# Kernel tuning notes

Measured on AMD Instinct MI355X. Metric: run time of the kernel, lower is better.

The kernel has to match this reference:

```python
import jax, jax.numpy as jnp
import numpy as np

B, C, D, H, W = 2, 32, 96, 96, 96
RED = 16
INV_SQRT2 = 0.7071067811865476  # 1/sqrt(2), Haar analysis filter coefficient
BN_EPS = 1e-5


def _haar1(x, axis):
    # pywt 'haar' DWT on even-length signals: a[i]=(x[2i]+x[2i+1])/sqrt2, d[i]=(x[2i]-x[2i+1])/sqrt2
    e = jax.lax.slice_in_dim(x, 0, None, stride=2, axis=axis)
    o = jax.lax.slice_in_dim(x, 1, None, stride=2, axis=axis)
    return (e + o) * INV_SQRT2, (e - o) * INV_SQRT2


def haar_dwt3d(x):
    # x: (B, C, D, H, W). Separable 3D Haar DWT; key letters follow pywt dwtn
    # axis order (D, H, W): 'aad' = approx along D, approx along H, detail along W.
    aD, dD = _haar1(x, 2)
    aa, ad = _haar1(aD, 3)
    da, dd = _haar1(dD, 3)
    aaa, aad = _haar1(aa, 4)
    ada, add = _haar1(ad, 4)
    daa, dad = _haar1(da, 4)
    dda, ddd = _haar1(dd, 4)
    # per-channel grouping of 7 detail bands, then flatten to (B, 7C, D/2, H/2, W/2)
    high = jnp.stack([aad, ada, add, daa, dad, dda, ddd], axis=2)
    b, c = x.shape[0], x.shape[1]
    high = high.reshape(b, c * 7, *aaa.shape[2:])
    return aaa, high


def chan_attn(x, w1, w2):
    # AdaptiveAvgPool3d(1) -> FC(no bias) -> ReLU -> FC(no bias) -> Sigmoid -> scale
    y = x.mean(axis=(2, 3, 4))                     # (B, Ch)
    y = jax.nn.sigmoid(jnp.maximum(y @ w1.T, 0.0) @ w2.T)
    return x * y[:, :, None, None, None]


def setup_inputs() -> dict:
    key = jax.random.key(0)
    ks = jax.random.split(key, 7)
    x = jax.random.normal(ks[0], (B, C, D, H, W), dtype=jnp.float32)
    w1_low = jax.random.normal(ks[1], (C // RED, C), dtype=jnp.float32) * 0.1
    w2_low = jax.random.normal(ks[2], (C, C // RED), dtype=jnp.float32) * 0.1
    w1_high = jax.random.normal(ks[3], (7 * C // RED, 7 * C), dtype=jnp.float32) * 0.05
    w2_high = jax.random.normal(ks[4], (7 * C, 7 * C // RED), dtype=jnp.float32) * 0.05
    w_fuse = jax.random.normal(ks[5], (C, 8 * C), dtype=jnp.float32) * 0.05  # 1x1x1 conv kernel
    b_fuse = jnp.zeros((C,), dtype=jnp.float32)
    gamma = jnp.ones((C,), dtype=jnp.float32)
    beta = jnp.zeros((C,), dtype=jnp.float32)
    return dict(x=x, w1_low=w1_low, w2_low=w2_low, w1_high=w1_high, w2_high=w2_high,
                w_fuse=w_fuse, b_fuse=b_fuse, gamma=gamma, beta=beta)


def reference(x, w1_low, w2_low, w1_high, w2_high, w_fuse, b_fuse, gamma, beta):
    low, high = haar_dwt3d(x)                                  # (B,C,48,48,48), (B,7C,48,48,48)
    low = chan_attn(low, w1_low, w2_low)
    high = chan_attn(high, w1_high, w2_high)
    z = jnp.concatenate([low, high], axis=1)                   # (B, 8C, 48,48,48)
    z = jnp.einsum('bcdhw,oc->bodhw', z, w_fuse) + b_fuse[None, :, None, None, None]
    # BatchNorm3d (training-mode batch statistics, as fresh torch module defaults)
    mu = z.mean(axis=(0, 2, 3, 4), keepdims=True)
    var = z.var(axis=(0, 2, 3, 4), keepdims=True)
    z = (z - mu) * jax.lax.rsqrt(var + BN_EPS)
    z = z * gamma[None, :, None, None, None] + beta[None, :, None, None, None]
    return jnp.maximum(z, 0.0)
```

## Files before the change

### kernel.cpp

```cpp
#include <hip/hip_runtime.h>
#include <math.h>

#define HS 0.35355339059327373f
#define NSPAT 110592
#define NBN   221184

__global__ __launch_bounds__(256) void k1_parity(const float* __restrict__ x,
                                                 float* __restrict__ S) {
    int blk = blockIdx.x;
    int d   = blk % 96;
    int bc  = blk / 96;
    const float4* x4 = (const float4*)x + (long)blk * 2304;
    int tid = threadIdx.x;
    float aE0 = 0.f, aO0 = 0.f, aE1 = 0.f, aO1 = 0.f;
#pragma unroll
    for (int i = 0; i < 9; ++i) {
        int f = tid + i * 256;
        float4 v = x4[f];
        int h = f / 24;
        float e = v.x + v.z, o = v.y + v.w;
        if (h & 1) { aE1 += e; aO1 += o; }
        else       { aE0 += e; aO0 += o; }
    }
#pragma unroll
    for (int m = 32; m; m >>= 1) {
        aE0 += __shfl_xor(aE0, m, 64); aO0 += __shfl_xor(aO0, m, 64);
        aE1 += __shfl_xor(aE1, m, 64); aO1 += __shfl_xor(aO1, m, 64);
    }
    __shared__ float red[4][4];
    int lane = tid & 63, wave = tid >> 6;
    if (lane == 0) { red[wave][0] = aE0; red[wave][1] = aO0;
                     red[wave][2] = aE1; red[wave][3] = aO1; }
    __syncthreads();
    if (tid < 4) {
        float v = red[0][tid] + red[1][tid] + red[2][tid] + red[3][tid];
        int q = tid >> 1, r = tid & 1, p = d & 1;
        atomicAdd(&S[bc * 8 + p * 4 + q * 2 + r], v);
    }
}

__global__ __launch_bounds__(256) void k2_attn(
        const float* __restrict__ S,
        const float* __restrict__ w1l, const float* __restrict__ w2l,
        const float* __restrict__ w1h, const float* __restrict__ w2h,
        const float* __restrict__ wf, float* __restrict__ A) {
    int b = blockIdx.x, tid = threadIdx.x;
    __shared__ float mlow[32], mhigh[224], h1l[2], h1h[14], ylow[32], yhigh[224];
    const float* Sb = S + b * 256;
    const float MS = HS / (float)NSPAT;
    if (tid < 32) {
        float s = 0.f;
        for (int j = 0; j < 8; ++j) s += Sb[tid * 8 + j];
        mlow[tid] = s * MS;
    }
    if (tid < 224) {
        int c = tid / 7, k = tid % 7, dm = k + 1;
        float s = 0.f;
        for (int j = 0; j < 8; ++j) {
            float sg = (__popc(j & dm) & 1) ? -1.f : 1.f;
            s += sg * Sb[c * 8 + j];
        }
        mhigh[tid] = s * MS;
    }
    __syncthreads();
    if (tid < 2) {
        float s = 0.f;
        for (int c = 0; c < 32; ++c) s += w1l[tid * 32 + c] * mlow[c];
        h1l[tid] = fmaxf(s, 0.f);
    } else if (tid < 16) {
        int j = tid - 2;
        float s = 0.f;
        for (int c = 0; c < 224; ++c) s += w1h[j * 224 + c] * mhigh[c];
        h1h[j] = fmaxf(s, 0.f);
    }
    __syncthreads();
    if (tid < 32) {
        float s = w2l[tid * 2] * h1l[0] + w2l[tid * 2 + 1] * h1l[1];
        ylow[tid] = 1.f / (1.f + expf(-s));
    } else if (tid < 256) {
        int i = tid - 32;
        float s = 0.f;
        for (int j = 0; j < 14; ++j) s += w2h[i * 14 + j] * h1h[j];
        yhigh[i] = 1.f / (1.f + expf(-s));
    }
    __syncthreads();
    for (int idx = tid; idx < 8192; idx += 256) {
        int o = idx >> 8, c = (idx >> 3) & 31, pqr = idx & 7;
        float a = wf[o * 256 + c] * ylow[c];
#pragma unroll
        for (int k = 0; k < 7; ++k) {
            float sg = (__popc(pqr & (k + 1)) & 1) ? -1.f : 1.f;
            a += sg * wf[o * 256 + 32 + c * 7 + k] * yhigh[c * 7 + k];
        }
        A[b * 8192 + c * 256 + o * 8 + pqr] = a * HS;
    }
}

__global__ __launch_bounds__(256) void k3_main(const float* __restrict__ x,
                                               const float* __restrict__ A,
                                               float* __restrict__ z,
                                               float* __restrict__ bnRep) {
    __shared__ float lds[4 * 64 * 33];
    int blk  = blockIdx.x;
    int vblk = blk % 36;
    int tmp  = blk / 36;
    int od   = tmp % 48;
    int b    = tmp / 48;
    int tid  = threadIdx.x;
    int lane = tid & 63;
    int wv   = __builtin_amdgcn_readfirstlane(tid >> 6);
    int vbase = vblk * 64;
    int v    = vbase + lane;
    int oh   = v / 48, ow = v % 48;

    const float* Ab = A + b * 8192;

    float acc[32];
#pragma unroll
    for (int o = 0; o < 32; ++o) acc[o] = 0.f;

    const float2* x2 = (const float2*)x;
    int base = (b * 32 + wv * 8) * 442368 + od * 9216 + oh * 96 + ow;

    float2 v00 = x2[base], v01 = x2[base + 48];
    float2 v10 = x2[base + 4608], v11 = x2[base + 4656];
#pragma unroll
    for (int i = 0; i < 8; ++i) {
        float2 n00, n01, n10, n11;
        if (i < 7) {
            int nb = base + (i + 1) * 442368;
            n00 = x2[nb]; n01 = x2[nb + 48];
            n10 = x2[nb + 4608]; n11 = x2[nb + 4656];
        }
        const float* Ac = Ab + (wv * 8 + i) * 256;
#pragma unroll
        for (int o = 0; o < 32; ++o) {
            const float* Ao = Ac + o * 8;
            acc[o] += Ao[0] * v00.x + Ao[1] * v00.y + Ao[2] * v01.x + Ao[3] * v01.y
                    + Ao[4] * v10.x + Ao[5] * v10.y + Ao[6] * v11.x + Ao[7] * v11.y;
        }
        if (i < 7) { v00 = n00; v01 = n01; v10 = n10; v11 = n11; }
    }

    float* mine = &lds[(wv * 64 + lane) * 33];
#pragma unroll
    for (int o = 0; o < 32; ++o) mine[o] = acc[o];
    __syncthreads();

    int o = tid >> 3, g = tid & 7;
    float val[8];
#pragma unroll
    for (int j = 0; j < 8; ++j) {
        int a0 = (g * 8 + j) * 33 + o;
        val[j] = lds[a0] + lds[2112 + a0] + lds[4224 + a0] + lds[6336 + a0];
    }
    int zf = ((b * 32 + o) * 48 + od) * 2304 + vbase + g * 8;
    float4* z4 = (float4*)(z + zf);
    z4[0] = make_float4(val[0], val[1], val[2], val[3]);
    z4[1] = make_float4(val[4], val[5], val[6], val[7]);

    float sv = 0.f, qv = 0.f;
#pragma unroll
    for (int j = 0; j < 8; ++j) { sv += val[j]; qv += val[j] * val[j]; }
#pragma unroll
    for (int m = 1; m <= 4; m <<= 1) {
        sv += __shfl_xor(sv, m, 64);
        qv += __shfl_xor(qv, m, 64);
    }
    if ((tid & 7) == 0) {
        int rep = (blockIdx.x & 15) * 64;
        atomicAdd(&bnRep[rep + o], sv);
        atomicAdd(&bnRep[rep + 32 + o], qv);
    }
}

__global__ __launch_bounds__(256) void k5_norm(float* __restrict__ z,
                                               const float* __restrict__ bnRep,
                                               const float* __restrict__ gamma,
                                               const float* __restrict__ beta) {
    __shared__ float s_sc[32], s_sh[32];
    int tid = threadIdx.x;
    if (tid < 32) {
        float s = 0.f, q = 0.f;
#pragma unroll
        for (int r = 0; r < 16; ++r) {
            s += bnRep[r * 64 + tid];
            q += bnRep[r * 64 + 32 + tid];
        }
        const float invN = 1.f / (float)NBN;
        float mean = s * invN;
        float var  = q * invN - mean * mean;
        float inv  = rsqrtf(var + 1e-5f);
        float sc   = gamma[tid] * inv;
        s_sc[tid] = sc;
        s_sh[tid] = beta[tid] - mean * sc;
    }
    int i = blockIdx.x * 256 + tid;
    float4* z4 = (float4*)z;
    float4 v = z4[i];
    __syncthreads();
    int o = (i / 27648) & 31;
    float sc = s_sc[o], sh = s_sh[o];
    v.x = fmaxf(v.x * sc + sh, 0.f);
    v.y = fmaxf(v.y * sc + sh, 0.f);
    v.z = fmaxf(v.z * sc + sh, 0.f);
    v.w = fmaxf(v.w * sc + sh, 0.f);
    z4[i] = v;
}

extern "C" void kernel_launch(void* const* d_in, const int* in_sizes, int n_in,
                              void* d_out, int out_size, void* d_ws, size_t ws_size,
                              hipStream_t stream) {
    const float* x    = (const float*)d_in[0];
    const float* w1l  = (const float*)d_in[1];
    const float* w2l  = (const float*)d_in[2];
    const float* w1h  = (const float*)d_in[3];
    const float* w2h  = (const float*)d_in[4];
    const float* wf   = (const float*)d_in[5];
    const float* gamma = (const float*)d_in[7];
    const float* beta  = (const float*)d_in[8];
    float* out = (float*)d_out;

    float* ws    = (float*)d_ws;
    float* S     = ws;
    float* bnRep = ws + 512;
    float* A     = ws + 2048;

    hipMemsetAsync(d_ws, 0, 1536 * sizeof(float), stream);
    k1_parity<<<6144, 256, 0, stream>>>(x, S);
    k2_attn<<<2, 256, 0, stream>>>(S, w1l, w2l, w1h, w2h, wf, A);
    k3_main<<<3456, 256, 0, stream>>>(x, A, out, bnRep);
    k5_norm<<<6912, 256, 0, stream>>>(out, bnRep, gamma, beta);
}
```

Measured before the change: 493.0 us.

## Split fused conv across waves by output channel instead of input channel

The main kernel now gives each wave 8 output channels over all 32 input channels, rather than 8 input channels over all 32 outputs. This removes the LDS cross-wave reduction, its __syncthreads, and the 32-element accumulator array, and the attention-weight table is re-laid out so each wave reads a contiguous block. In exchange, every wave loads the full set of input samples, so global load instructions per block rise fourfold, relying on the cache to absorb the repeats. The batch-norm partial sums also now use full-wave shuffle reductions per output channel.

```diff
diff --git a/kernel.cpp b/kernel.cpp
--- a/kernel.cpp
+++ b/kernel.cpp
@@ -92,7 +92,8 @@
             float sg = (__popc(pqr & (k + 1)) & 1) ? -1.f : 1.f;
             a += sg * wf[o * 256 + 32 + c * 7 + k] * yhigh[c * 7 + k];
         }
-        A[b * 8192 + c * 256 + o * 8 + pqr] = a * HS;
+        int og = o >> 3, op = o & 7;
+        A[b * 8192 + og * 2048 + c * 64 + op * 8 + pqr] = a * HS;
     }
 }
 
@@ -100,7 +101,6 @@
                                                const float* __restrict__ A,
                                                float* __restrict__ z,
                                                float* __restrict__ bnRep) {
-    __shared__ float lds[4 * 64 * 33];
     int blk  = blockIdx.x;
     int vblk = blk % 36;
     int tmp  = blk / 36;
@@ -109,68 +109,56 @@
     int tid  = threadIdx.x;
     int lane = tid & 63;
     int wv   = __builtin_amdgcn_readfirstlane(tid >> 6);
-    int vbase = vblk * 64;
-    int v    = vbase + lane;
+    int v    = vblk * 64 + lane;
     int oh   = v / 48, ow = v % 48;
 
-    const float* Ab = A + b * 8192;
-
-    float acc[32];
-#pragma unroll
-    for (int o = 0; o < 32; ++o) acc[o] = 0.f;
+    const float* Ab = A + b * 8192 + wv * 2048;
+
+    float acc[8];
+#pragma unroll
+    for (int o = 0; o < 8; ++o) acc[o] = 0.f;
 
     const float2* x2 = (const float2*)x;
-    int base = (b * 32 + wv * 8) * 442368 + od * 9216 + oh * 96 + ow;
-
-    float2 v00 = x2[base], v01 = x2[base + 48];
+    int base = (b * 32) * 442368 + od * 9216 + oh * 96 + ow;
+
+    float2 v00 = x2[base],        v01 = x2[base + 48];
     float2 v10 = x2[base + 4608], v11 = x2[base + 4656];
-#pragma unroll
-    for (int i = 0; i < 8; ++i) {
+    for (int c = 0; c < 32; ++c) {
         float2 n00, n01, n10, n11;
-        if (i < 7) {
-            int nb = base + (i + 1) * 442368;
-            n00 = x2[nb]; n01 = x2[nb + 48];
+        if (c < 31) {
+            int nb = base + (c + 1) * 442368;
+            n00 = x2[nb];        n01 = x2[nb + 48];
             n10 = x2[nb + 4608]; n11 = x2[nb + 4656];
         }
-        const float* Ac = Ab + (wv * 8 + i) * 256;
-#pragma unroll
-        for (int o = 0; o < 32; ++o) {
+        const float* Ac = Ab + c * 64;
+#pragma unroll
+        for (int o = 0; o < 8; ++o) {
             const float* Ao = Ac + o * 8;
             acc[o] += Ao[0] * v00.x + Ao[1] * v00.y + Ao[2] * v01.x + Ao[3] * v01.y
                     + Ao[4] * v10.x + Ao[5] * v10.y + Ao[6] * v11.x + Ao[7] * v11.y;
         }
-        if (i < 7) { v00 = n00; v01 = n01; v10 = n10; v11 = n11; }
-    }
-
-    float* mine = &lds[(wv * 64 + lane) * 33];
-#pragma unroll
-    for (int o = 0; o < 32; ++o) mine[o] = acc[o];
-    __syncthreads();
-
-    int o = tid >> 3, g = tid & 7;
-    float val[8];
-#pragma unroll
-    for (int j = 0; j < 8; ++j) {
-        int a0 = (g * 8 + j) * 33 + o;
-        val[j] = lds[a0] + lds[2112 + a0] + lds[4224 + a0] + lds[6336 + a0];
-    }
-    int zf = ((b * 32 + o) * 48 + od) * 2304 + vbase + g * 8;
-    float4* z4 = (float4*)(z + zf);
-    z4[0] = make_float4(val[0], val[1], val[2], val[3]);
-    z4[1] = make_float4(val[4], val[5], val[6], val[7]);
-
-    float sv = 0.f, qv = 0.f;
-#pragma unroll
-    for (int j = 0; j < 8; ++j) { sv += val[j]; qv += val[j] * val[j]; }
-#pragma unroll
-    for (int m = 1; m <= 4; m <<= 1) {
-        sv += __shfl_xor(sv, m, 64);
-        qv += __shfl_xor(qv, m, 64);
-    }
-    if ((tid & 7) == 0) {
-        int rep = (blockIdx.x & 15) * 64;
-        atomicAdd(&bnRep[rep + o], sv);
-        atomicAdd(&bnRep[rep + 32 + o], qv);
+        v00 = n00; v01 = n01; v10 = n10; v11 = n11;
+    }
+
+#pragma unroll
+    for (int o = 0; o < 8; ++o) {
+        z[((b * 32 + wv * 8 + o) * 48 + od) * 2304 + v] = acc[o];
+    }
+
+    int rep = (blockIdx.x & 15) * 64;
+#pragma unroll
+    for (int o = 0; o < 8; ++o) {
+        float sv = acc[o];
+        float qv = acc[o] * acc[o];
+#pragma unroll
+        for (int m = 32; m; m >>= 1) {
+            sv += __shfl_xor(sv, m, 64);
+            qv += __shfl_xor(qv, m, 64);
+        }
+        if (lane == 0) {
+            atomicAdd(&bnRep[rep + wv * 8 + o], sv);
+            atomicAdd(&bnRep[rep + 32 + wv * 8 + o], qv);
+        }
     }
 }
 
```

Result: faster. 469.9 us (-4.7%).
